# Kernel tuning notes

Hardware: AMD Instinct MI355X
Metric: run time of the kernel (lower is better)

## Reference

```python
import jax, jax.numpy as jnp
import numpy as np

B, T, D_IN, H, D_OUT, MLP_H = 512, 1024, 64, 256, 64, 256


def setup_inputs() -> dict:
    key = jax.random.key(0)
    ks = jax.random.split(key, 12)
    s_ih = 1.0 / np.sqrt(H)
    return {
        "x": jax.random.normal(ks[0], (B, T, D_IN), dtype=jnp.float32),
        "mask": jax.random.uniform(ks[1], (B, T, 1), dtype=jnp.float32),
        "h0": jax.random.normal(ks[2], (B, H), dtype=jnp.float32),
        "c0": jax.random.normal(ks[3], (B, H), dtype=jnp.float32),
        # LSTMCell params (PyTorch layout: gates in i, f, g, o order)
        "W_ih": jax.random.uniform(ks[4], (4 * H, D_IN), minval=-s_ih, maxval=s_ih, dtype=jnp.float32),
        "W_hh": jax.random.uniform(ks[5], (4 * H, H), minval=-s_ih, maxval=s_ih, dtype=jnp.float32),
        "b_ih": jax.random.uniform(ks[6], (4 * H,), minval=-s_ih, maxval=s_ih, dtype=jnp.float32),
        "b_hh": jax.random.uniform(ks[7], (4 * H,), minval=-s_ih, maxval=s_ih, dtype=jnp.float32),
        # output MLP: Linear(H, MLP_H) -> ReLU -> Linear(MLP_H, D_OUT)
        "W1": jax.random.normal(ks[8], (MLP_H, H), dtype=jnp.float32) * (1.0 / np.sqrt(H)),
        "b1": jnp.zeros((MLP_H,), dtype=jnp.float32),
        "W2": jax.random.normal(ks[9], (D_OUT, MLP_H), dtype=jnp.float32) * (1.0 / np.sqrt(MLP_H)),
        "b2": jnp.zeros((D_OUT,), dtype=jnp.float32),
    }


def _lstm_scan(x, h0, c0, W_ih, W_hh, b_ih, b_hh):
    # precompute input projections for all timesteps: [T, B, 4H]
    x_tb = jnp.swapaxes(x, 0, 1)  # [T, B, D_IN]
    x_proj = jnp.einsum("tbd,gd->tbg", x_tb, W_ih) + b_ih + b_hh

    def step(carry, xp):
        h, c = carry
        gates = xp + h @ W_hh.T  # [B, 4H]
        i, f, g, o = jnp.split(gates, 4, axis=-1)
        i = jax.nn.sigmoid(i)
        f = jax.nn.sigmoid(f)
        g = jnp.tanh(g)
        o = jax.nn.sigmoid(o)
        c = f * c + i * g
        h = o * jnp.tanh(c)
        return (h, c), h

    _, hs = jax.lax.scan(step, (h0, c0), x_proj)  # hs: [T, B, H]
    return jnp.swapaxes(hs, 0, 1)  # [B, T, H]


def reference(x, mask, h0, c0, W_ih, W_hh, b_ih, b_hh, W1, b1, W2, b2):
    hs = _lstm_scan(x, h0, c0, W_ih, W_hh, b_ih, b_hh)  # [B, T, H]
    y = jax.nn.relu(hs @ W1.T + b1) @ W2.T + b2  # [B, T, D_OUT]
    return y * mask
```

## Files before the change

### kernel.cpp

```cpp
#include <hip/hip_runtime.h>
#include <stdint.h>
#include <stddef.h>

#define T_STEPS 1024
#define BATCH   512
#define HID     256
#define DIN     64

typedef __attribute__((ext_vector_type(8))) short short8;
typedef __attribute__((ext_vector_type(4))) short short4v;
typedef __attribute__((ext_vector_type(2))) short short2v;
typedef __attribute__((ext_vector_type(4))) float float4v;

static __device__ __forceinline__ short f2bf(float f) {
  union { float f; unsigned u; } v; v.f = f;
  unsigned r = (v.u + 0x7FFFu + ((v.u >> 16) & 1u)) >> 16;
  return (short)r;
}
static __device__ __forceinline__ float sigm(float x) {
  return 1.0f / (1.0f + __expf(-x));
}
static __device__ __forceinline__ float tanh_f(float x) {
  return 2.0f / (1.0f + __expf(-2.0f * x)) - 1.0f;
}

static __device__ __forceinline__ void ast64x2_l2(unsigned long long* p,
                                                  unsigned long long v0,
                                                  unsigned long long v1) {
  asm volatile("global_atomic_swap_x2 %0, %1, off\n\t"
               "global_atomic_swap_x2 %0, %2, off offset:8"
               :: "v"(p), "v"(v0), "v"(v1) : "memory");
}
static __device__ __forceinline__ void ald64x2_l2(const unsigned long long* p,
                                                  unsigned long long& r0,
                                                  unsigned long long& r1) {
  unsigned long long z = 0;
  asm volatile("global_atomic_add_x2 %0, %2, %3, off sc0\n\t"
               "global_atomic_add_x2 %1, %2, %3, off offset:8 sc0\n\t"
               "s_waitcnt vmcnt(0)"
               : "=&v"(r0), "=&v"(r1)
               : "v"(p), "v"(z)
               : "memory");
}

__global__ __launch_bounds__(512, 2) void lstm_kernel(
    const float* __restrict__ x, const float* __restrict__ h0,
    const float* __restrict__ c0, const float* __restrict__ W_ih,
    const float* __restrict__ W_hh, const float* __restrict__ b_ih,
    const float* __restrict__ b_hh, float* __restrict__ exch,
    float* __restrict__ exchf, unsigned* __restrict__ tbl,
    uint16_t* __restrict__ hs) {
  const int tid   = threadIdx.x;
  const int blk   = blockIdx.x;
  const int group = blk & 31;
  const int half  = blk >> 5;
  const int b0    = group * 16;
  const int w     = tid >> 6;
  const int lane  = tid & 63;
  const int quad  = lane >> 4;
  const int l16   = lane & 15;
  const int partner = blk ^ 32;

  __shared__ short Alds[16 * 328];
  __shared__ float Glds[16 * 516];
  __shared__ int s_fastex;

  const int urow = tid >> 5;
  const int hh0  = (tid & 31) * 4;
  const int xc   = (tid & 31) * 2;

  const int widx = urow * 64 + (hh0 >> 1);
  unsigned long long* sbuf[2];
  const unsigned long long* pbuf[2];
  unsigned long long* sfast[2];
  const unsigned long long* pfast[2];
#pragma unroll
  for (int bfi = 0; bfi < 2; ++bfi) {
    sbuf[bfi]  = (unsigned long long*)(exch + ((size_t)blk * 2 + bfi) * 2048) + widx;
    pbuf[bfi]  = (const unsigned long long*)(exch + ((size_t)partner * 2 + bfi) * 2048) + widx;
    sfast[bfi] = (unsigned long long*)exchf + ((size_t)blk * 2 + bfi) * 1024 + widx;
    pfast[bfi] = (const unsigned long long*)exchf + ((size_t)partner * 2 + bfi) * 1024 + widx;
  }

  if (tid == 0) {
    int xcd;
    asm volatile("s_getreg_b32 %0, hwreg(HW_REG_XCC_ID)" : "=s"(xcd));
    unsigned my = 0x5AB00000u | ((unsigned)xcd & 0xFFu);
    __hip_atomic_store(&tbl[blk], my, __ATOMIC_RELAXED, __HIP_MEMORY_SCOPE_AGENT);
    unsigned pv = 0;
    for (int g2 = 0; g2 < (1 << 16); ++g2) {
      pv = __hip_atomic_load(&tbl[partner], __ATOMIC_RELAXED, __HIP_MEMORY_SCOPE_AGENT);
      if ((pv & 0xFFFFFF00u) == 0x5AB00000u) break;
      __builtin_amdgcn_s_sleep(8);
    }
    s_fastex = (((pv & 0xFFFFFF00u) == 0x5AB00000u) &&
                ((pv & 0xFFu) == (my & 0xFFu))) ? 1 : 0;
  }

  short8 bw[10][4];
#pragma unroll
  for (int j = 0; j < 10; ++j) {
    int ktA = (j < 4) ? (half * 4 + j) : (j < 8) ? ((1 - half) * 4 + (j - 4)) : j;
#pragma unroll
    for (int nt = 0; nt < 4; ++nt) {
      int n_loc = w * 64 + nt * 16 + l16;
      int gate  = n_loc >> 7;
      int hh    = n_loc & 127;
      int grow  = gate * 256 + half * 128 + hh;
      const float* src = (ktA < 8)
          ? (W_hh + (size_t)grow * 256 + ktA * 32 + quad * 8)
          : (W_ih + (size_t)grow * 64 + (ktA - 8) * 32 + quad * 8);
      short8 bv;
#pragma unroll
      for (int e = 0; e < 8; ++e) bv[e] = f2bf(src[e]);
      bw[j][nt] = bv;
    }
  }

  float bias[4][4];
  float c_reg[4];
#pragma unroll
  for (int g = 0; g < 4; ++g) {
    const float* bi = b_ih + g * 256 + half * 128 + hh0;
    const float* bh = b_hh + g * 256 + half * 128 + hh0;
#pragma unroll
    for (int r = 0; r < 4; ++r) bias[g][r] = bi[r] + bh[r];
  }
  {
    const float* c0p = c0 + (size_t)(b0 + urow) * 256 + half * 128 + hh0;
#pragma unroll
    for (int r = 0; r < 4; ++r) c_reg[r] = c0p[r];
  }

  {
    int c8 = (tid & 31) * 8;
    const float* hp = h0 + (size_t)(b0 + urow) * 256 + c8;
    short8 hv;
#pragma unroll
    for (int e = 0; e < 8; ++e) hv[e] = f2bf(hp[e]);
    *(short8*)&Alds[urow * 328 + c8] = hv;
    const float* xp = x + ((size_t)(b0 + urow) * T_STEPS + 0) * DIN + xc;
    short2v xv2; xv2[0] = f2bf(xp[0]); xv2[1] = f2bf(xp[1]);
    *(short2v*)&Alds[urow * 328 + 256 + xc] = xv2;
  }
  __syncthreads();
  const int fastex = s_fastex;

  const int ownbase = half * 128;
  const int pbase   = (1 - half) * 128;

  for (int t = 0; t < T_STEPS; ++t) {
    float4v acc[4] = {{0.f,0.f,0.f,0.f},{0.f,0.f,0.f,0.f},
                      {0.f,0.f,0.f,0.f},{0.f,0.f,0.f,0.f}};
    int tn = (t + 1 < T_STEPS) ? (t + 1) : t;
    const float* xp = x + ((size_t)(b0 + urow) * T_STEPS + tn) * DIN + xc;
    float xa = xp[0], xb = xp[1];

#pragma unroll
    for (int j = 0; j < 4; ++j) {
      short8 a = *(const short8*)&Alds[l16 * 328 + ownbase + j * 32 + quad * 8];
#pragma unroll
      for (int nt = 0; nt < 4; ++nt)
        acc[nt] = __builtin_amdgcn_mfma_f32_16x16x32_bf16(a, bw[j][nt], acc[nt], 0, 0, 0);
    }
#pragma unroll
    for (int j = 8; j < 10; ++j) {
      short8 a = *(const short8*)&Alds[l16 * 328 + 256 + (j - 8) * 32 + quad * 8];
#pragma unroll
      for (int nt = 0; nt < 4; ++nt)
        acc[nt] = __builtin_amdgcn_mfma_f32_16x16x32_bf16(a, bw[j][nt], acc[nt], 0, 0, 0);
    }

    if (t > 0) {
      int buf = (t - 1) & 1;
      short4v pv4;
      if (fastex) {
        unsigned idw = 0xC0DE0000u + (unsigned)(t - 1);
        unsigned long long w0 = 0, w1 = 0;
        int guard = 0;
        for (;;) {
          ald64x2_l2(pfast[buf], w0, w1);
          if (((unsigned)w0 == idw) & ((unsigned)(w1 >> 32) == idw)) break;
          if (++guard > 1024) break;
        }
        unsigned pay01 = (unsigned)(w0 >> 32);
        unsigned pay23 = (unsigned)w1;
        pv4[0] = (short)(pay01 & 0xFFFFu); pv4[1] = (short)(pay01 >> 16);
        pv4[2] = (short)(pay23 & 0xFFFFu); pv4[3] = (short)(pay23 >> 16);
      } else {
        unsigned tag = 1u ^ (((unsigned)(t - 1) >> 1) & 1u);
        const unsigned long long* p = pbuf[buf];
        unsigned long long w0, w1;
        int guard = 0;
        for (;;) {
          w0 = __hip_atomic_load(p,     __ATOMIC_RELAXED, __HIP_MEMORY_SCOPE_AGENT);
          w1 = __hip_atomic_load(p + 1, __ATOMIC_RELAXED, __HIP_MEMORY_SCOPE_AGENT);
          bool ok = (((unsigned)w0 & 1u) == tag) & ((((unsigned)(w0 >> 32)) & 1u) == tag) &
                    (((unsigned)w1 & 1u) == tag) & ((((unsigned)(w1 >> 32)) & 1u) == tag);
          if (ok) break;
          if (++guard > 4096) break;
        }
        union { unsigned u; float f; } g0, g1, g2, g3;
        g0.u = (unsigned)w0; g1.u = (unsigned)(w0 >> 32);
        g2.u = (unsigned)w1; g3.u = (unsigned)(w1 >> 32);
        pv4[0] = f2bf(g0.f); pv4[1] = f2bf(g1.f);
        pv4[2] = f2bf(g2.f); pv4[3] = f2bf(g3.f);
      }
      *(short4v*)&Alds[urow * 328 + pbase + hh0] = pv4;
    }
    __syncthreads();

#pragma unroll
    for (int j = 4; j < 8; ++j) {
      short8 a = *(const short8*)&Alds[l16 * 328 + pbase + (j - 4) * 32 + quad * 8];
#pragma unroll
      for (int nt = 0; nt < 4; ++nt)
        acc[nt] = __builtin_amdgcn_mfma_f32_16x16x32_bf16(a, bw[j][nt], acc[nt], 0, 0, 0);
    }
#pragma unroll
    for (int nt = 0; nt < 4; ++nt) {
      int col = w * 64 + nt * 16 + l16;
#pragma unroll
      for (int r = 0; r < 4; ++r)
        Glds[(quad * 4 + r) * 516 + col] = acc[nt][r];
    }
    __syncthreads();

    float4v ip = *(const float4v*)&Glds[urow * 516 + 0   + hh0];
    float4v fp = *(const float4v*)&Glds[urow * 516 + 128 + hh0];
    float4v gp = *(const float4v*)&Glds[urow * 516 + 256 + hh0];
    float4v op = *(const float4v*)&Glds[urow * 516 + 384 + hh0];
    float hf[4];
    short hb[4];
#pragma unroll
    for (int r = 0; r < 4; ++r) {
      float iv = sigm(ip[r] + bias[0][r]);
      float fv = sigm(fp[r] + bias[1][r]);
      float gv = tanh_f(gp[r] + bias[2][r]);
      float ov = sigm(op[r] + bias[3][r]);
      float cv = fv * c_reg[r] + iv * gv;
      c_reg[r] = cv;
      hf[r] = ov * tanh_f(cv);
      hb[r] = f2bf(hf[r]);
    }
    {
      int buf = t & 1;
      if (fastex) {
        unsigned idw = 0xC0DE0000u + (unsigned)t;
        unsigned pay01 = (unsigned)(unsigned short)hb[0]
                       | ((unsigned)(unsigned short)hb[1] << 16);
        unsigned pay23 = (unsigned)(unsigned short)hb[2]
                       | ((unsigned)(unsigned short)hb[3] << 16);
        unsigned long long w0 = (unsigned long long)idw
                              | ((unsigned long long)pay01 << 32);
        unsigned long long w1 = (unsigned long long)pay23
                              | ((unsigned long long)idw << 32);
        ast64x2_l2(sfast[buf], w0, w1);
      } else {
        unsigned tag = 1u ^ (((unsigned)t >> 1) & 1u);
        union { float f; unsigned u; } u0, u1, u2, u3;
        u0.f = hf[0]; u1.f = hf[1]; u2.f = hf[2]; u3.f = hf[3];
        unsigned long long w0 = (unsigned long long)((u0.u & ~1u) | tag)
                              | ((unsigned long long)((u1.u & ~1u) | tag) << 32);
        unsigned long long w1 = (unsigned long long)((u2.u & ~1u) | tag)
                              | ((unsigned long long)((u3.u & ~1u) | tag) << 32);
        __hip_atomic_store(sbuf[buf],     w0, __ATOMIC_RELAXED, __HIP_MEMORY_SCOPE_AGENT);
        __hip_atomic_store(sbuf[buf] + 1, w1, __ATOMIC_RELAXED, __HIP_MEMORY_SCOPE_AGENT);
      }
    }
    short4v hv4; hv4[0] = hb[0]; hv4[1] = hb[1]; hv4[2] = hb[2]; hv4[3] = hb[3];
    *(short4v*)&Alds[urow * 328 + ownbase + hh0] = hv4;
    *(short4v*)(hs + ((size_t)(b0 + urow) * T_STEPS + t) * HID + ownbase + hh0) = hv4;
    short2v xv2; xv2[0] = f2bf(xa); xv2[1] = f2bf(xb);
    *(short2v*)&Alds[urow * 328 + 256 + xc] = xv2;
    __syncthreads();
  }
}

__global__ void prep_kernel(const float* __restrict__ W1, const float* __restrict__ W2,
                            short* __restrict__ W1b, short* __restrict__ W2b,
                            unsigned* __restrict__ tbl) {
  int i = blockIdx.x * 512 + threadIdx.x;
  if (i < 64)
    __hip_atomic_store(&tbl[i], 0u, __ATOMIC_RELAXED, __HIP_MEMORY_SCOPE_AGENT);
  if (i < 65536) W1b[i] = f2bf(W1[i]);
  else           W2b[i - 65536] = f2bf(W2[i - 65536]);
}

__global__ __launch_bounds__(512, 2) void mlp_kernel(
    const uint16_t* __restrict__ hs, const short* __restrict__ W1b,
    const float* __restrict__ b1, const short* __restrict__ W2b,
    const float* __restrict__ b2, const float* __restrict__ mask,
    float* __restrict__ y) {
  const int tid   = threadIdx.x;
  const int rows0 = blockIdx.x * 128;
  const int w     = tid >> 6;
  const int lane  = tid & 63;
  const int quad  = lane >> 4;
  const int l16   = lane & 15;

  __shared__ short S[128 * 264];

#pragma unroll
  for (int kk = 0; kk < 8; ++kk) {
    int c   = tid + kk * 512;
    int row = c >> 5;
    int off = (c & 31) * 8;
    *(short8*)&S[row * 264 + off] =
        *(const short8*)(hs + (size_t)(rows0 + row) * HID + off);
  }

  short8 bf1[2][8];
  float  b1v[2];
#pragma unroll
  for (int nt = 0; nt < 2; ++nt) {
    int n = w * 32 + nt * 16 + l16;
    b1v[nt] = b1[n];
#pragma unroll
    for (int kt = 0; kt < 8; ++kt)
      bf1[nt][kt] = *(const short8*)(W1b + (size_t)n * 256 + kt * 32 + quad * 8);
  }
  __syncthreads();

  float4v acc1[2][8];
#pragma unroll
  for (int nt = 0; nt < 2; ++nt)
#pragma unroll
    for (int mt = 0; mt < 8; ++mt) acc1[nt][mt] = (float4v){0.f,0.f,0.f,0.f};
#pragma unroll
  for (int kt = 0; kt < 8; ++kt) {
#pragma unroll
    for (int mt = 0; mt < 8; ++mt) {
      short8 a = *(const short8*)&S[(mt * 16 + l16) * 264 + kt * 32 + quad * 8];
#pragma unroll
      for (int nt = 0; nt < 2; ++nt)
        acc1[nt][mt] = __builtin_amdgcn_mfma_f32_16x16x32_bf16(a, bf1[nt][kt], acc1[nt][mt], 0, 0, 0);
    }
  }
  __syncthreads();

#pragma unroll
  for (int nt = 0; nt < 2; ++nt) {
    int col = w * 32 + nt * 16 + l16;
#pragma unroll
    for (int mt = 0; mt < 8; ++mt)
#pragma unroll
      for (int r = 0; r < 4; ++r) {
        float v = acc1[nt][mt][r] + b1v[nt];
        v = v > 0.f ? v : 0.f;
        S[(mt * 16 + quad * 4 + r) * 264 + col] = f2bf(v);
      }
  }
  __syncthreads();

  const int mt2 = w >> 1;
  short8 a2[8];
#pragma unroll
  for (int kt = 0; kt < 8; ++kt)
    a2[kt] = *(const short8*)(W2b + (size_t)(mt2 * 16 + l16) * 256 + kt * 32 + quad * 8);
  float4v acc2[4] = {{0.f,0.f,0.f,0.f},{0.f,0.f,0.f,0.f},
                     {0.f,0.f,0.f,0.f},{0.f,0.f,0.f,0.f}};
#pragma unroll
  for (int kt = 0; kt < 8; ++kt) {
#pragma unroll
    for (int nt2 = 0; nt2 < 4; ++nt2) {
      int n0 = (w & 1) * 64 + nt2 * 16;
      short8 b = *(const short8*)&S[(n0 + l16) * 264 + kt * 32 + quad * 8];
      acc2[nt2] = __builtin_amdgcn_mfma_f32_16x16x32_bf16(a2[kt], b, acc2[nt2], 0, 0, 0);
    }
  }
  const float* b2p = b2 + mt2 * 16 + quad * 4;
  float b2v0 = b2p[0], b2v1 = b2p[1], b2v2 = b2p[2], b2v3 = b2p[3];
#pragma unroll
  for (int nt2 = 0; nt2 < 4; ++nt2) {
    int R = rows0 + (w & 1) * 64 + nt2 * 16 + l16;
    float m = mask[R];
    float4v out;
    out[0] = (acc2[nt2][0] + b2v0) * m;
    out[1] = (acc2[nt2][1] + b2v1) * m;
    out[2] = (acc2[nt2][2] + b2v2) * m;
    out[3] = (acc2[nt2][3] + b2v3) * m;
    *(float4v*)(y + (size_t)R * 64 + mt2 * 16 + quad * 4) = out;
  }
}

extern "C" void kernel_launch(void* const* d_in, const int* in_sizes, int n_in,
                              void* d_out, int out_size, void* d_ws, size_t ws_size,
                              hipStream_t stream) {
  (void)in_sizes; (void)n_in; (void)out_size; (void)ws_size;
  const float* x    = (const float*)d_in[0];
  const float* mask = (const float*)d_in[1];
  const float* h0   = (const float*)d_in[2];
  const float* c0   = (const float*)d_in[3];
  const float* W_ih = (const float*)d_in[4];
  const float* W_hh = (const float*)d_in[5];
  const float* b_ih = (const float*)d_in[6];
  const float* b_hh = (const float*)d_in[7];
  const float* W1   = (const float*)d_in[8];
  const float* b1   = (const float*)d_in[9];
  const float* W2   = (const float*)d_in[10];
  const float* b2   = (const float*)d_in[11];
  float* y = (float*)d_out;

  char* ws = (char*)d_ws;
  float*    exch  = (float*)ws;
  float*    exchf = (float*)(ws + (1u << 20));
  short*    W1b   = (short*)(ws + (2u << 20));
  short*    W2b   = (short*)(ws + (2u << 20) + 131072);
  unsigned* tbl   = (unsigned*)(ws + (2u << 20) + 131072 + 32768);
  uint16_t* hs    = (uint16_t*)(ws + (3u << 20));

  prep_kernel<<<160, 512, 0, stream>>>(W1, W2, W1b, W2b, tbl);
  lstm_kernel<<<64, 512, 0, stream>>>(x, h0, c0, W_ih, W_hh, b_ih, b_hh, exch, exchf, tbl, hs);
  mlp_kernel<<<4096, 512, 0, stream>>>(hs, W1b, b1, W2b, b2, mask, y);
}
```

Before: 3.682 ms.

## Remap gate columns so MFMA accumulators hold all four gates per lane

Weight columns are reassigned so each wave's four MFMA accumulators hold the i, f, g and o gates for the same hidden units. Gate activations can then be computed straight from registers. This removes the Glds staging buffer, its scatter writes and reads, and one __syncthreads per timestep. The hs store is deferred one step and done from LDS in the vectorised layout, and the exchange indexing is changed to match the new per-lane ownership. The cost is scalar 2-byte LDS writes of h, which may cause bank conflicts.

Result: faster. 3.404 ms (-7.6%).

```diff
diff --git a/kernel.cpp b/kernel.cpp
--- a/kernel.cpp
+++ b/kernel.cpp
@@ -59,17 +59,17 @@
   const int lane  = tid & 63;
   const int quad  = lane >> 4;
   const int l16   = lane & 15;
+  const int w16l  = w * 16 + l16;
   const int partner = blk ^ 32;
 
   __shared__ short Alds[16 * 328];
-  __shared__ float Glds[16 * 516];
   __shared__ int s_fastex;
 
   const int urow = tid >> 5;
   const int hh0  = (tid & 31) * 4;
   const int xc   = (tid & 31) * 2;
 
-  const int widx = urow * 64 + (hh0 >> 1);
+  const int widx = tid * 2;
   unsigned long long* sbuf[2];
   const unsigned long long* pbuf[2];
   unsigned long long* sfast[2];
@@ -102,35 +102,29 @@
   for (int j = 0; j < 10; ++j) {
     int ktA = (j < 4) ? (half * 4 + j) : (j < 8) ? ((1 - half) * 4 + (j - 4)) : j;
 #pragma unroll
-    for (int nt = 0; nt < 4; ++nt) {
-      int n_loc = w * 64 + nt * 16 + l16;
-      int gate  = n_loc >> 7;
-      int hh    = n_loc & 127;
-      int grow  = gate * 256 + half * 128 + hh;
+    for (int g = 0; g < 4; ++g) {
+      int n_loc = g * 128 + w16l;
+      int grow  = g * 256 + half * 128 + w16l;
       const float* src = (ktA < 8)
           ? (W_hh + (size_t)grow * 256 + ktA * 32 + quad * 8)
           : (W_ih + (size_t)grow * 64 + (ktA - 8) * 32 + quad * 8);
+      (void)n_loc;
       short8 bv;
 #pragma unroll
       for (int e = 0; e < 8; ++e) bv[e] = f2bf(src[e]);
-      bw[j][nt] = bv;
-    }
-  }
-
-  float bias[4][4];
+      bw[j][g] = bv;
+    }
+  }
+
+  const int hh_abs = half * 128 + w16l;
+  float bias_g[4];
+#pragma unroll
+  for (int g = 0; g < 4; ++g)
+    bias_g[g] = b_ih[g * 256 + hh_abs] + b_hh[g * 256 + hh_abs];
   float c_reg[4];
 #pragma unroll
-  for (int g = 0; g < 4; ++g) {
-    const float* bi = b_ih + g * 256 + half * 128 + hh0;
-    const float* bh = b_hh + g * 256 + half * 128 + hh0;
-#pragma unroll
-    for (int r = 0; r < 4; ++r) bias[g][r] = bi[r] + bh[r];
-  }
-  {
-    const float* c0p = c0 + (size_t)(b0 + urow) * 256 + half * 128 + hh0;
-#pragma unroll
-    for (int r = 0; r < 4; ++r) c_reg[r] = c0p[r];
-  }
+  for (int r = 0; r < 4; ++r)
+    c_reg[r] = c0[(size_t)(b0 + quad * 4 + r) * 256 + hh_abs];
 
   {
     int c8 = (tid & 31) * 8;
@@ -160,15 +154,20 @@
     for (int j = 0; j < 4; ++j) {
       short8 a = *(const short8*)&Alds[l16 * 328 + ownbase + j * 32 + quad * 8];
 #pragma unroll
-      for (int nt = 0; nt < 4; ++nt)
-        acc[nt] = __builtin_amdgcn_mfma_f32_16x16x32_bf16(a, bw[j][nt], acc[nt], 0, 0, 0);
+      for (int g = 0; g < 4; ++g)
+        acc[g] = __builtin_amdgcn_mfma_f32_16x16x32_bf16(a, bw[j][g], acc[g], 0, 0, 0);
     }
 #pragma unroll
     for (int j = 8; j < 10; ++j) {
       short8 a = *(const short8*)&Alds[l16 * 328 + 256 + (j - 8) * 32 + quad * 8];
 #pragma unroll
-      for (int nt = 0; nt < 4; ++nt)
-        acc[nt] = __builtin_amdgcn_mfma_f32_16x16x32_bf16(a, bw[j][nt], acc[nt], 0, 0, 0);
+      for (int g = 0; g < 4; ++g)
+        acc[g] = __builtin_amdgcn_mfma_f32_16x16x32_bf16(a, bw[j][g], acc[g], 0, 0, 0);
+    }
+
+    if (t > 0) {
+      short4v hv = *(const short4v*)&Alds[urow * 328 + ownbase + hh0];
+      *(short4v*)(hs + ((size_t)(b0 + urow) * T_STEPS + (t - 1)) * HID + ownbase + hh0) = hv;
     }
 
     if (t > 0) {
@@ -206,7 +205,9 @@
         pv4[0] = f2bf(g0.f); pv4[1] = f2bf(g1.f);
         pv4[2] = f2bf(g2.f); pv4[3] = f2bf(g3.f);
       }
-      *(short4v*)&Alds[urow * 328 + pbase + hh0] = pv4;
+#pragma unroll
+      for (int r = 0; r < 4; ++r)
+        Alds[(quad * 4 + r) * 328 + pbase + w16l] = pv4[r];
     }
     __syncthreads();
 
@@ -214,30 +215,18 @@
     for (int j = 4; j < 8; ++j) {
       short8 a = *(const short8*)&Alds[l16 * 328 + pbase + (j - 4) * 32 + quad * 8];
 #pragma unroll
-      for (int nt = 0; nt < 4; ++nt)
-        acc[nt] = __builtin_amdgcn_mfma_f32_16x16x32_bf16(a, bw[j][nt], acc[nt], 0, 0, 0);
-    }
-#pragma unroll
-    for (int nt = 0; nt < 4; ++nt) {
-      int col = w * 64 + nt * 16 + l16;
-#pragma unroll
-      for (int r = 0; r < 4; ++r)
-        Glds[(quad * 4 + r) * 516 + col] = acc[nt][r];
-    }
-    __syncthreads();
-
-    float4v ip = *(const float4v*)&Glds[urow * 516 + 0   + hh0];
-    float4v fp = *(const float4v*)&Glds[urow * 516 + 128 + hh0];
-    float4v gp = *(const float4v*)&Glds[urow * 516 + 256 + hh0];
-    float4v op = *(const float4v*)&Glds[urow * 516 + 384 + hh0];
+      for (int g = 0; g < 4; ++g)
+        acc[g] = __builtin_amdgcn_mfma_f32_16x16x32_bf16(a, bw[j][g], acc[g], 0, 0, 0);
+    }
+
     float hf[4];
     short hb[4];
 #pragma unroll
     for (int r = 0; r < 4; ++r) {
-      float iv = sigm(ip[r] + bias[0][r]);
-      float fv = sigm(fp[r] + bias[1][r]);
-      float gv = tanh_f(gp[r] + bias[2][r]);
-      float ov = sigm(op[r] + bias[3][r]);
+      float iv = sigm(acc[0][r] + bias_g[0]);
+      float fv = sigm(acc[1][r] + bias_g[1]);
+      float gv = tanh_f(acc[2][r] + bias_g[2]);
+      float ov = sigm(acc[3][r] + bias_g[3]);
       float cv = fv * c_reg[r] + iv * gv;
       c_reg[r] = cv;
       hf[r] = ov * tanh_f(cv);
@@ -268,12 +257,17 @@
         __hip_atomic_store(sbuf[buf] + 1, w1, __ATOMIC_RELAXED, __HIP_MEMORY_SCOPE_AGENT);
       }
     }
-    short4v hv4; hv4[0] = hb[0]; hv4[1] = hb[1]; hv4[2] = hb[2]; hv4[3] = hb[3];
-    *(short4v*)&Alds[urow * 328 + ownbase + hh0] = hv4;
-    *(short4v*)(hs + ((size_t)(b0 + urow) * T_STEPS + t) * HID + ownbase + hh0) = hv4;
+#pragma unroll
+    for (int r = 0; r < 4; ++r)
+      Alds[(quad * 4 + r) * 328 + ownbase + w16l] = hb[r];
     short2v xv2; xv2[0] = f2bf(xa); xv2[1] = f2bf(xb);
     *(short2v*)&Alds[urow * 328 + 256 + xc] = xv2;
     __syncthreads();
+  }
+
+  {
+    short4v hv = *(const short4v*)&Alds[urow * 328 + ownbase + hh0];
+    *(short4v*)(hs + ((size_t)(b0 + urow) * T_STEPS + (T_STEPS - 1)) * HID + ownbase + hh0) = hv;
   }
 }
 
```
